# Optimization experiments

Hardware: AMD Instinct MI355X
Metric: run time of the kernel (lower is better)

Reference implementation:

```python
import jax, jax.numpy as jnp
import numpy as np

WIN_H, WIN_W = 8, 8
NUM_HEADS = 32


def _relative_position_index(wh: int, ww: int) -> np.ndarray:
    # Swin V1 style pairwise relative position index, [wh*ww, wh*ww]
    coords = np.stack(np.meshgrid(np.arange(wh), np.arange(ww), indexing='ij'))  # [2, wh, ww]
    cf = coords.reshape(2, -1)                      # [2, N]
    rel = cf[:, :, None] - cf[:, None, :]           # [2, N, N]
    rel = rel.transpose(1, 2, 0).copy()             # [N, N, 2]
    rel[:, :, 0] += wh - 1
    rel[:, :, 1] += ww - 1
    rel[:, :, 0] *= 2 * ww - 1
    return rel.sum(-1)                              # [N, N]


def setup_inputs() -> dict:
    key = jax.random.key(0)
    ks = jax.random.split(key, 6)
    B, N, C = 2048, WIN_H * WIN_W, 256
    return {
        'x': jax.random.normal(ks[0], (B, N, C), dtype=jnp.float32),
        'w_qkv': jax.random.normal(ks[1], (3 * C, C), dtype=jnp.float32) * 0.02,
        'b_qkv': jax.random.normal(ks[2], (3 * C,), dtype=jnp.float32) * 0.02,
        'w_proj': jax.random.normal(ks[3], (C, C), dtype=jnp.float32) * 0.02,
        'b_proj': jax.random.normal(ks[4], (C,), dtype=jnp.float32) * 0.02,
        'bias_table': jax.random.normal(ks[5], ((2 * WIN_H - 1) * (2 * WIN_W - 1), NUM_HEADS), dtype=jnp.float32) * 0.02,
    }


def reference(x, w_qkv, b_qkv, w_proj, b_proj, bias_table):
    B, N, C = x.shape
    H = NUM_HEADS
    d = C // H
    idx = jnp.asarray(_relative_position_index(WIN_H, WIN_W).reshape(-1))  # [N*N] int
    # gathered relative positional bias: [H, N, N]
    bias = bias_table[idx].reshape(N, N, H).transpose(2, 0, 1)
    # qkv projection -> [3, B, H, N, d]
    qkv = (x @ w_qkv.T + b_qkv).reshape(B, N, 3, H, d).transpose(2, 0, 3, 1, 4)
    q, k, v = qkv[0], qkv[1], qkv[2]
    # NOTE: torch code normalizes over dim=1 == HEAD axis (faithful quirk),
    # and self.scale is never applied in forward.
    def norm_heads(t):
        n = jnp.sqrt(jnp.sum(t * t, axis=1, keepdims=True))
        return t / jnp.maximum(n, 1e-12)
    q = norm_heads(q)
    k = norm_heads(k)
    logits = jnp.einsum('bhqd,bhkd->bhqk', q, k) + bias[None]  # [B,H,N,N]
    attn = jax.nn.softmax(logits, axis=-1)
    out = jnp.einsum('bhqk,bhkd->bhqd', attn, v)               # [B,H,N,d]
    out = out.transpose(0, 2, 1, 3).reshape(B, N, C)
    return out @ w_proj.T + b_proj
```

## Files before the change

kernel.cpp:

```cpp
#include <hip/hip_runtime.h>

typedef __attribute__((ext_vector_type(4))) float f32x4;
typedef __attribute__((ext_vector_type(8))) short s16x8;
typedef __attribute__((ext_vector_type(4))) short s16x4;

#define NWIN 2048
#define NTOK 64
#define CDIM 256
#define NHEAD 32

__device__ __forceinline__ ushort f2bf(float f) {
    union { float f; unsigned u; } v; v.f = f;
    unsigned r = v.u + 0x7FFFu + ((v.u >> 16) & 1u);
    return (ushort)(r >> 16);
}
__device__ __forceinline__ float bf2f(ushort u) {
    union { unsigned u; float f; } v; v.u = ((unsigned)u) << 16;
    return v.f;
}

__global__ void prep_kernel(const float* __restrict__ wqkv,
                            const float* __restrict__ wproj,
                            const float* __restrict__ btab,
                            ushort* __restrict__ wq,
                            ushort* __restrict__ wp,
                            ushort* __restrict__ bb) {
    int t = blockIdx.x * 256 + threadIdx.x;
    if (t < 196608) {
        wq[t] = f2bf(wqkv[t]);
    } else if (t < 262144) {
        int i = t - 196608;
        wp[i] = f2bf(wproj[i]);
    } else if (t < 393216) {
        int i = t - 262144;
        int h  = i >> 12;
        int rem = i & 4095;
        int qi = rem >> 6;
        int kj = rem & 63;
        int rh = (qi >> 3) - (kj >> 3) + 7;
        int rw = (qi & 7)  - (kj & 7)  + 7;
        bb[i] = f2bf(btab[(rh * 15 + rw) * 32 + h]);
    }
}

__global__ __launch_bounds__(512, 2) void attn_kernel(
    const float* __restrict__ x,
    const float* __restrict__ bqkv,
    const float* __restrict__ bproj,
    const ushort* __restrict__ wq,
    const ushort* __restrict__ wp,
    const ushort* __restrict__ biasb,
    float* __restrict__ out)
{
    __shared__ ushort sQ [NHEAD * NTOK * 8];
    __shared__ ushort sK [NHEAD * NTOK * 8];
    __shared__ ushort sVT[NHEAD * 8 * NTOK];
    __shared__ ushort sX [NTOK * CDIM];

    const int tid  = threadIdx.x;
    const int lane = tid & 63;
    const int w    = tid >> 6;
    const int g    = lane >> 4;
    const int c    = lane & 15;
    const int b    = blockIdx.x;

    const f32x4 fz = {0.f, 0.f, 0.f, 0.f};
    const s16x4 sz4 = {0, 0, 0, 0};

    {
        const float4* xg = (const float4*)(x + (size_t)b * (NTOK * CDIM));
        #pragma unroll
        for (int it = 0; it < 8; ++it) {
            int i = tid + it * 512;
            float4 v = xg[i];
            int row = i >> 6;
            int col = (i & 63) << 2;
            int bo = row * 512 + col * 2;
            bo ^= (row & 7) << 4;
            ushort4 u;
            u.x = f2bf(v.x); u.y = f2bf(v.y); u.z = f2bf(v.z); u.w = f2bf(v.w);
            *(ushort4*)((char*)sX + bo) = u;
        }
    }
    __syncthreads();

    {
        f32x4 acc[4][6];
        #pragma unroll
        for (int mi = 0; mi < 4; ++mi)
            #pragma unroll
            for (int nj = 0; nj < 6; ++nj) acc[mi][nj] = fz;

        #pragma unroll
        for (int ks = 0; ks < 8; ++ks) {
            s16x8 af[4];
            #pragma unroll
            for (int mi = 0; mi < 4; ++mi) {
                int row = 16 * mi + c;
                int bo = row * 512 + ks * 64 + g * 16;
                bo ^= (row & 7) << 4;
                af[mi] = *(const s16x8*)((const char*)sX + bo);
            }
            s16x8 wfr[6];
            #pragma unroll
            for (int nj = 0; nj < 6; ++nj) {
                int col = 96 * w + 16 * nj + c;
                wfr[nj] = *(const s16x8*)(wq + col * 256 + ks * 32 + g * 8);
            }
            #pragma unroll
            for (int mi = 0; mi < 4; ++mi)
                #pragma unroll
                for (int nj = 0; nj < 6; ++nj)
                    acc[mi][nj] = __builtin_amdgcn_mfma_f32_16x16x32_bf16(
                        af[mi], wfr[nj], acc[mi][nj], 0, 0, 0);
        }

        #pragma unroll
        for (int nj = 0; nj < 6; ++nj) {
            int col   = 96 * w + 16 * nj + c;
            int which = col >> 8;
            int hh    = (col >> 3) & 31;
            int dd    = col & 7;
            float bias = bqkv[col];
            #pragma unroll
            for (int mi = 0; mi < 4; ++mi) {
                #pragma unroll
                for (int j = 0; j < 4; ++j) {
                    int m = 16 * mi + 4 * g + j;
                    ushort bv = f2bf(acc[mi][nj][j] + bias);
                    if (which == 0)      sQ [(hh * 64 + m) * 8 + dd] = bv;
                    else if (which == 1) sK [(hh * 64 + m) * 8 + dd] = bv;
                    else                 sVT[(hh * 8 + dd) * 64 + m] = bv;
                }
            }
        }
    }
    __syncthreads();

    {
        float* sInv = (float*)sX;
        int n = tid >> 3, dd = tid & 7;
        float sq = 0.f, sk = 0.f;
        #pragma unroll 8
        for (int h = 0; h < 32; ++h) {
            float qv = bf2f(sQ[(h * 64 + n) * 8 + dd]);
            float kv = bf2f(sK[(h * 64 + n) * 8 + dd]);
            sq += qv * qv;
            sk += kv * kv;
        }
        sInv[tid]       = 1.f / fmaxf(sqrtf(sq), 1e-12f);
        sInv[512 + tid] = 1.f / fmaxf(sqrtf(sk), 1e-12f);
        __syncthreads();
        for (int r = tid; r < 2048; r += 512) {
            int h = r >> 6, nn = r & 63;
            ushort* qp = sQ + (h * 64 + nn) * 8;
            ushort* kp = sK + (h * 64 + nn) * 8;
            const float* iq = sInv + nn * 8;
            const float* ik = sInv + 512 + nn * 8;
            #pragma unroll
            for (int d2 = 0; d2 < 8; ++d2) {
                qp[d2] = f2bf(bf2f(qp[d2]) * iq[d2]);
                kp[d2] = f2bf(bf2f(kp[d2]) * ik[d2]);
            }
        }
    }
    __syncthreads();

    {
        #pragma unroll 1
        for (int hi = 0; hi < 4; ++hi) {
            int h = w * 4 + hi;
            s16x4 kf[4], qf[4];
            #pragma unroll
            for (int t = 0; t < 4; ++t) {
                if (g < 2) {
                    kf[t] = *(const s16x4*)(sK + (h * 64 + 16 * t + c) * 8 + g * 4);
                    qf[t] = *(const s16x4*)(sQ + (h * 64 + 16 * t + c) * 8 + g * 4);
                } else { kf[t] = sz4; qf[t] = sz4; }
            }
            f32x4 S[4][4];
            #pragma unroll
            for (int tk = 0; tk < 4; ++tk)
                #pragma unroll
                for (int tq = 0; tq < 4; ++tq)
                    S[tk][tq] = __builtin_amdgcn_mfma_f32_16x16x16bf16_1k(
                        kf[tk], qf[tq], fz, 0, 0, 0);

            const ushort* bh = biasb + h * 4096;
            float rinv[4];
            #pragma unroll
            for (int tq = 0; tq < 4; ++tq) {
                float sum = 0.f;
                #pragma unroll
                for (int tk = 0; tk < 4; ++tk) {
                    ushort4 bv4 = *(const ushort4*)(bh + (16 * tq + c) * 64 + 16 * tk + 4 * g);
                    float e0 = __expf(S[tk][tq][0] + bf2f(bv4.x));
                    float e1 = __expf(S[tk][tq][1] + bf2f(bv4.y));
                    float e2 = __expf(S[tk][tq][2] + bf2f(bv4.z));
                    float e3 = __expf(S[tk][tq][3] + bf2f(bv4.w));
                    S[tk][tq][0] = e0; S[tk][tq][1] = e1;
                    S[tk][tq][2] = e2; S[tk][tq][3] = e3;
                    sum += e0 + e1 + e2 + e3;
                }
                sum += __shfl_xor(sum, 16);
                sum += __shfl_xor(sum, 32);
                rinv[tq] = 1.f / sum;
            }

            s16x4 vf[4];
            #pragma unroll
            for (int kv = 0; kv < 4; ++kv) {
                if (c < 8) vf[kv] = *(const s16x4*)(sVT + (h * 8 + c) * 64 + 16 * kv + 4 * g);
                else vf[kv] = sz4;
            }
            f32x4 o[4];
            #pragma unroll
            for (int tq = 0; tq < 4; ++tq) o[tq] = fz;
            #pragma unroll
            for (int tq = 0; tq < 4; ++tq) {
                #pragma unroll
                for (int kv = 0; kv < 4; ++kv) {
                    s16x4 pa;
                    pa[0] = (short)f2bf(S[kv][tq][0] * rinv[tq]);
                    pa[1] = (short)f2bf(S[kv][tq][1] * rinv[tq]);
                    pa[2] = (short)f2bf(S[kv][tq][2] * rinv[tq]);
                    pa[3] = (short)f2bf(S[kv][tq][3] * rinv[tq]);
                    o[tq] = __builtin_amdgcn_mfma_f32_16x16x16bf16_1k(pa, vf[kv], o[tq], 0, 0, 0);
                }
            }
            if (c < 8) {
                #pragma unroll
                for (int tq = 0; tq < 4; ++tq) {
                    #pragma unroll
                    for (int j = 0; j < 4; ++j) {
                        int q = 16 * tq + 4 * g + j;
                        int bo = q * 512 + (h * 8 + c) * 2;
                        bo ^= (q & 7) << 4;
                        *(ushort*)((char*)sX + bo) = f2bf(o[tq][j]);
                    }
                }
            }
        }
    }
    __syncthreads();

    {
        f32x4 pacc[4][2];
        #pragma unroll
        for (int mi = 0; mi < 4; ++mi) { pacc[mi][0] = fz; pacc[mi][1] = fz; }

        #pragma unroll
        for (int ks = 0; ks < 8; ++ks) {
            s16x8 af[4];
            #pragma unroll
            for (int mi = 0; mi < 4; ++mi) {
                int row = 16 * mi + c;
                int bo = row * 512 + ks * 64 + g * 16;
                bo ^= (row & 7) << 4;
                af[mi] = *(const s16x8*)((const char*)sX + bo);
            }
            s16x8 wfr[2];
            #pragma unroll
            for (int nj = 0; nj < 2; ++nj) {
                int col = 32 * w + 16 * nj + c;
                wfr[nj] = *(const s16x8*)(wp + col * 256 + ks * 32 + g * 8);
            }
            #pragma unroll
            for (int mi = 0; mi < 4; ++mi)
                #pragma unroll
                for (int nj = 0; nj < 2; ++nj)
                    pacc[mi][nj] = __builtin_amdgcn_mfma_f32_16x16x32_bf16(
                        af[mi], wfr[nj], pacc[mi][nj], 0, 0, 0);
        }

        float* og = out + (size_t)b * (NTOK * CDIM);
        #pragma unroll
        for (int nj = 0; nj < 2; ++nj) {
            int col = 32 * w + 16 * nj + c;
            float bp = bproj[col];
            #pragma unroll
            for (int mi = 0; mi < 4; ++mi) {
                #pragma unroll
                for (int j = 0; j < 4; ++j) {
                    int row = 16 * mi + 4 * g + j;
                    og[row * 256 + col] = pacc[mi][nj][j] + bp;
                }
            }
        }
    }
}

extern "C" void kernel_launch(void* const* d_in, const int* in_sizes, int n_in,
                              void* d_out, int out_size, void* d_ws, size_t ws_size,
                              hipStream_t stream) {
    const float* x     = (const float*)d_in[0];
    const float* wqkv  = (const float*)d_in[1];
    const float* bqkv  = (const float*)d_in[2];
    const float* wproj = (const float*)d_in[3];
    const float* bproj = (const float*)d_in[4];
    const float* btab  = (const float*)d_in[5];

    ushort* wq_b   = (ushort*)d_ws;
    ushort* wp_b   = wq_b + 196608;
    ushort* bias_b = wp_b + 65536;

    prep_kernel<<<1536, 256, 0, stream>>>(wqkv, wproj, btab, wq_b, wp_b, bias_b);
    attn_kernel<<<NWIN, 512, 0, stream>>>(x, bqkv, bproj, wq_b, wp_b, bias_b,
                                          (float*)d_out);
}
```

Baseline: 361.0 us.

## Keep Q/K/V in registers and drop shared staging buffers

Q, K and V projections now stay in registers. Each wave computes the head slices it later consumes, with Q/K computed transposed so the accumulator layout matches the MFMA operand layout. The head-axis norm is accumulated with shared-memory atomicAdd into a small buffer, which removes the sQ/sK/sVT arrays and the separate normalisation pass with its extra barrier. The smaller LDS footprint allows launch bounds of 4 blocks per CU. The cost is higher register pressure from many live accumulators, plus LDS atomic contention.

```diff
diff --git a/kernel.cpp b/kernel.cpp
--- a/kernel.cpp
+++ b/kernel.cpp
@@ -5,9 +5,6 @@
 typedef __attribute__((ext_vector_type(4))) short s16x4;
 
 #define NWIN 2048
-#define NTOK 64
-#define CDIM 256
-#define NHEAD 32
 
 __device__ __forceinline__ ushort f2bf(float f) {
     union { float f; unsigned u; } v; v.f = f;
@@ -18,6 +15,10 @@
     union { unsigned u; float f; } v; v.u = ((unsigned)u) << 16;
     return v.f;
 }
+__device__ __forceinline__ unsigned pk2(float a, float b) {
+    return (unsigned)f2bf(a) | ((unsigned)f2bf(b) << 16);
+}
+union BF4 { unsigned u[2]; s16x4 v; };
 
 __global__ void prep_kernel(const float* __restrict__ wqkv,
                             const float* __restrict__ wproj,
@@ -43,7 +44,7 @@
     }
 }
 
-__global__ __launch_bounds__(512, 2) void attn_kernel(
+__global__ __launch_bounds__(512, 4) void attn_kernel(
     const float* __restrict__ x,
     const float* __restrict__ bqkv,
     const float* __restrict__ bproj,
@@ -52,10 +53,8 @@
     const ushort* __restrict__ biasb,
     float* __restrict__ out)
 {
-    __shared__ ushort sQ [NHEAD * NTOK * 8];
-    __shared__ ushort sK [NHEAD * NTOK * 8];
-    __shared__ ushort sVT[NHEAD * 8 * NTOK];
-    __shared__ ushort sX [NTOK * CDIM];
+    __shared__ ushort sX[64 * 256];
+    __shared__ float  sN[1024];
 
     const int tid  = threadIdx.x;
     const int lane = tid & 63;
@@ -65,18 +64,19 @@
     const int b    = blockIdx.x;
 
     const f32x4 fz = {0.f, 0.f, 0.f, 0.f};
-    const s16x4 sz4 = {0, 0, 0, 0};
+    const s16x4 z4 = {0, 0, 0, 0};
+
+    sN[tid] = 0.f; sN[tid + 512] = 0.f;
 
     {
-        const float4* xg = (const float4*)(x + (size_t)b * (NTOK * CDIM));
+        const float4* xg = (const float4*)(x + (size_t)b * 16384);
         #pragma unroll
         for (int it = 0; it < 8; ++it) {
             int i = tid + it * 512;
             float4 v = xg[i];
             int row = i >> 6;
             int col = (i & 63) << 2;
-            int bo = row * 512 + col * 2;
-            bo ^= (row & 7) << 4;
+            int bo = (row * 512 + col * 2) ^ ((row & 7) << 4);
             ushort4 u;
             u.x = f2bf(v.x); u.y = f2bf(v.y); u.z = f2bf(v.z); u.w = f2bf(v.w);
             *(ushort4*)((char*)sX + bo) = u;
@@ -84,159 +84,170 @@
     }
     __syncthreads();
 
+    unsigned vpku[4][2][2];
     {
-        f32x4 acc[4][6];
-        #pragma unroll
-        for (int mi = 0; mi < 4; ++mi)
-            #pragma unroll
-            for (int nj = 0; nj < 6; ++nj) acc[mi][nj] = fz;
-
+        f32x4 acc[4][2];
+        #pragma unroll
+        for (int mi = 0; mi < 4; ++mi) { acc[mi][0] = fz; acc[mi][1] = fz; }
         #pragma unroll
         for (int ks = 0; ks < 8; ++ks) {
             s16x8 af[4];
             #pragma unroll
             for (int mi = 0; mi < 4; ++mi) {
                 int row = 16 * mi + c;
-                int bo = row * 512 + ks * 64 + g * 16;
-                bo ^= (row & 7) << 4;
+                int bo = (row * 512 + ks * 64 + g * 16) ^ ((row & 7) << 4);
                 af[mi] = *(const s16x8*)((const char*)sX + bo);
             }
-            s16x8 wfr[6];
-            #pragma unroll
-            for (int nj = 0; nj < 6; ++nj) {
-                int col = 96 * w + 16 * nj + c;
-                wfr[nj] = *(const s16x8*)(wq + col * 256 + ks * 32 + g * 8);
-            }
+            s16x8 wv[2];
+            #pragma unroll
+            for (int nj = 0; nj < 2; ++nj)
+                wv[nj] = *(const s16x8*)(wq + (512 + 32 * w + 16 * nj + c) * 256 + ks * 32 + g * 8);
             #pragma unroll
             for (int mi = 0; mi < 4; ++mi)
                 #pragma unroll
-                for (int nj = 0; nj < 6; ++nj)
-                    acc[mi][nj] = __builtin_amdgcn_mfma_f32_16x16x32_bf16(
-                        af[mi], wfr[nj], acc[mi][nj], 0, 0, 0);
-        }
-
-        #pragma unroll
-        for (int nj = 0; nj < 6; ++nj) {
-            int col   = 96 * w + 16 * nj + c;
-            int which = col >> 8;
-            int hh    = (col >> 3) & 31;
-            int dd    = col & 7;
-            float bias = bqkv[col];
-            #pragma unroll
-            for (int mi = 0; mi < 4; ++mi) {
-                #pragma unroll
-                for (int j = 0; j < 4; ++j) {
-                    int m = 16 * mi + 4 * g + j;
-                    ushort bv = f2bf(acc[mi][nj][j] + bias);
-                    if (which == 0)      sQ [(hh * 64 + m) * 8 + dd] = bv;
-                    else if (which == 1) sK [(hh * 64 + m) * 8 + dd] = bv;
-                    else                 sVT[(hh * 8 + dd) * 64 + m] = bv;
+                for (int nj = 0; nj < 2; ++nj)
+                    acc[mi][nj] = __builtin_amdgcn_mfma_f32_16x16x32_bf16(af[mi], wv[nj], acc[mi][nj], 0, 0, 0);
+        }
+        float bv[2];
+        bv[0] = bqkv[512 + 32 * w + c];
+        bv[1] = bqkv[512 + 32 * w + 16 + c];
+        #pragma unroll
+        for (int mi = 0; mi < 4; ++mi)
+            #pragma unroll
+            for (int nj = 0; nj < 2; ++nj) {
+                vpku[mi][nj][0] = pk2(acc[mi][nj][0] + bv[nj], acc[mi][nj][1] + bv[nj]);
+                vpku[mi][nj][1] = pk2(acc[mi][nj][2] + bv[nj], acc[mi][nj][3] + bv[nj]);
+            }
+    }
+
+    f32x4 aq[2][4], ak[2][4];
+    {
+        #pragma unroll
+        for (int mt = 0; mt < 2; ++mt)
+            #pragma unroll
+            for (int nt = 0; nt < 4; ++nt) { aq[mt][nt] = fz; ak[mt][nt] = fz; }
+        #pragma unroll
+        for (int ks = 0; ks < 8; ++ks) {
+            s16x8 af[4];
+            #pragma unroll
+            for (int nt = 0; nt < 4; ++nt) {
+                int row = 16 * nt + c;
+                int bo = (row * 512 + ks * 64 + g * 16) ^ ((row & 7) << 4);
+                af[nt] = *(const s16x8*)((const char*)sX + bo);
+            }
+            s16x8 wqa[2], wka[2];
+            #pragma unroll
+            for (int mt = 0; mt < 2; ++mt) {
+                wqa[mt] = *(const s16x8*)(wq + (32 * w + 16 * mt + c) * 256 + ks * 32 + g * 8);
+                wka[mt] = *(const s16x8*)(wq + (256 + 32 * w + 16 * mt + c) * 256 + ks * 32 + g * 8);
+            }
+            #pragma unroll
+            for (int mt = 0; mt < 2; ++mt)
+                #pragma unroll
+                for (int nt = 0; nt < 4; ++nt) {
+                    aq[mt][nt] = __builtin_amdgcn_mfma_f32_16x16x32_bf16(wqa[mt], af[nt], aq[mt][nt], 0, 0, 0);
+                    ak[mt][nt] = __builtin_amdgcn_mfma_f32_16x16x32_bf16(wka[mt], af[nt], ak[mt][nt], 0, 0, 0);
                 }
-            }
-        }
+        }
+        f32x4 bq[2], bk[2];
+        bq[0] = *(const f32x4*)(bqkv + 32 * w + 4 * g);
+        bq[1] = *(const f32x4*)(bqkv + 32 * w + 16 + 4 * g);
+        bk[0] = *(const f32x4*)(bqkv + 256 + 32 * w + 4 * g);
+        bk[1] = *(const f32x4*)(bqkv + 256 + 32 * w + 16 + 4 * g);
+        #pragma unroll
+        for (int mt = 0; mt < 2; ++mt)
+            #pragma unroll
+            for (int nt = 0; nt < 4; ++nt) { aq[mt][nt] += bq[mt]; ak[mt][nt] += bk[mt]; }
+        #pragma unroll
+        for (int nt = 0; nt < 4; ++nt)
+            #pragma unroll
+            for (int j = 0; j < 4; ++j) {
+                int a = (16 * nt + c) * 8 + ((4 * g + j) & 7);
+                atomicAdd(&sN[a],       aq[0][nt][j] * aq[0][nt][j] + aq[1][nt][j] * aq[1][nt][j]);
+                atomicAdd(&sN[a + 512], ak[0][nt][j] * ak[0][nt][j] + ak[1][nt][j] * ak[1][nt][j]);
+            }
     }
     __syncthreads();
 
-    {
-        float* sInv = (float*)sX;
-        int n = tid >> 3, dd = tid & 7;
-        float sq = 0.f, sk = 0.f;
-        #pragma unroll 8
-        for (int h = 0; h < 32; ++h) {
-            float qv = bf2f(sQ[(h * 64 + n) * 8 + dd]);
-            float kv = bf2f(sK[(h * 64 + n) * 8 + dd]);
-            sq += qv * qv;
-            sk += kv * kv;
-        }
-        sInv[tid]       = 1.f / fmaxf(sqrtf(sq), 1e-12f);
-        sInv[512 + tid] = 1.f / fmaxf(sqrtf(sk), 1e-12f);
-        __syncthreads();
-        for (int r = tid; r < 2048; r += 512) {
-            int h = r >> 6, nn = r & 63;
-            ushort* qp = sQ + (h * 64 + nn) * 8;
-            ushort* kp = sK + (h * 64 + nn) * 8;
-            const float* iq = sInv + nn * 8;
-            const float* ik = sInv + 512 + nn * 8;
-            #pragma unroll
-            for (int d2 = 0; d2 < 8; ++d2) {
-                qp[d2] = f2bf(bf2f(qp[d2]) * iq[d2]);
-                kp[d2] = f2bf(bf2f(kp[d2]) * ik[d2]);
-            }
-        }
-    }
-    __syncthreads();
-
-    {
-        #pragma unroll 1
-        for (int hi = 0; hi < 4; ++hi) {
-            int h = w * 4 + hi;
-            s16x4 kf[4], qf[4];
-            #pragma unroll
-            for (int t = 0; t < 4; ++t) {
-                if (g < 2) {
-                    kf[t] = *(const s16x4*)(sK + (h * 64 + 16 * t + c) * 8 + g * 4);
-                    qf[t] = *(const s16x4*)(sQ + (h * 64 + 16 * t + c) * 8 + g * 4);
-                } else { kf[t] = sz4; qf[t] = sz4; }
-            }
-            f32x4 S[4][4];
-            #pragma unroll
-            for (int tk = 0; tk < 4; ++tk)
-                #pragma unroll
-                for (int tq = 0; tq < 4; ++tq)
-                    S[tk][tq] = __builtin_amdgcn_mfma_f32_16x16x16bf16_1k(
-                        kf[tk], qf[tq], fz, 0, 0, 0);
-
-            const ushort* bh = biasb + h * 4096;
-            float rinv[4];
-            #pragma unroll
-            for (int tq = 0; tq < 4; ++tq) {
+    s16x4 qpk[2][4], kpk[2][4];
+    #pragma unroll
+    for (int nt = 0; nt < 4; ++nt) {
+        float iq[4], ik[4];
+        #pragma unroll
+        for (int j = 0; j < 4; ++j) {
+            int a = (16 * nt + c) * 8 + ((4 * g + j) & 7);
+            iq[j] = 1.f / fmaxf(sqrtf(sN[a]), 1e-12f);
+            ik[j] = 1.f / fmaxf(sqrtf(sN[a + 512]), 1e-12f);
+        }
+        #pragma unroll
+        for (int mt = 0; mt < 2; ++mt) {
+            BF4 uq, uk;
+            uq.u[0] = pk2(aq[mt][nt][0] * iq[0], aq[mt][nt][1] * iq[1]);
+            uq.u[1] = pk2(aq[mt][nt][2] * iq[2], aq[mt][nt][3] * iq[3]);
+            uk.u[0] = pk2(ak[mt][nt][0] * ik[0], ak[mt][nt][1] * ik[1]);
+            uk.u[1] = pk2(ak[mt][nt][2] * ik[2], ak[mt][nt][3] * ik[3]);
+            qpk[mt][nt] = uq.v; kpk[mt][nt] = uk.v;
+        }
+    }
+
+    #pragma unroll
+    for (int hi = 0; hi < 4; ++hi) {
+        const int mt = hi >> 1, par = hi & 1, h = 4 * w + hi;
+        const bool keepq = par ? (g >= 2) : (g < 2);
+        s16x4 vf[4];
+        #pragma unroll
+        for (int kv = 0; kv < 4; ++kv) {
+            unsigned u0 = vpku[kv][mt][0], u1 = vpku[kv][mt][1];
+            if (par) { u0 = (unsigned)__shfl_xor((int)u0, 8); u1 = (unsigned)__shfl_xor((int)u1, 8); }
+            BF4 t; t.u[0] = u0; t.u[1] = u1;
+            vf[kv] = (c < 8) ? t.v : z4;
+        }
+        const ushort* bh = biasb + h * 4096;
+        #pragma unroll
+        for (int tqh = 0; tqh < 2; ++tqh) {
+            f32x4 S[4][2];
+            #pragma unroll
+            for (int t2 = 0; t2 < 2; ++t2) {
+                s16x4 qf = keepq ? qpk[mt][2 * tqh + t2] : z4;
+                #pragma unroll
+                for (int tk = 0; tk < 4; ++tk)
+                    S[tk][t2] = __builtin_amdgcn_mfma_f32_16x16x16bf16_1k(kpk[mt][tk], qf, fz, 0, 0, 0);
+            }
+            float rinv[2];
+            #pragma unroll
+            for (int t2 = 0; t2 < 2; ++t2) {
                 float sum = 0.f;
                 #pragma unroll
                 for (int tk = 0; tk < 4; ++tk) {
-                    ushort4 bv4 = *(const ushort4*)(bh + (16 * tq + c) * 64 + 16 * tk + 4 * g);
-                    float e0 = __expf(S[tk][tq][0] + bf2f(bv4.x));
-                    float e1 = __expf(S[tk][tq][1] + bf2f(bv4.y));
-                    float e2 = __expf(S[tk][tq][2] + bf2f(bv4.z));
-                    float e3 = __expf(S[tk][tq][3] + bf2f(bv4.w));
-                    S[tk][tq][0] = e0; S[tk][tq][1] = e1;
-                    S[tk][tq][2] = e2; S[tk][tq][3] = e3;
+                    ushort4 bv4 = *(const ushort4*)(bh + (16 * (2 * tqh + t2) + c) * 64 + 16 * tk + 4 * g);
+                    float e0 = __expf(S[tk][t2][0] + bf2f(bv4.x));
+                    float e1 = __expf(S[tk][t2][1] + bf2f(bv4.y));
+                    float e2 = __expf(S[tk][t2][2] + bf2f(bv4.z));
+                    float e3 = __expf(S[tk][t2][3] + bf2f(bv4.w));
+                    S[tk][t2][0] = e0; S[tk][t2][1] = e1;
+                    S[tk][t2][2] = e2; S[tk][t2][3] = e3;
                     sum += e0 + e1 + e2 + e3;
                 }
                 sum += __shfl_xor(sum, 16);
                 sum += __shfl_xor(sum, 32);
-                rinv[tq] = 1.f / sum;
-            }
-
-            s16x4 vf[4];
-            #pragma unroll
-            for (int kv = 0; kv < 4; ++kv) {
-                if (c < 8) vf[kv] = *(const s16x4*)(sVT + (h * 8 + c) * 64 + 16 * kv + 4 * g);
-                else vf[kv] = sz4;
-            }
-            f32x4 o[4];
-            #pragma unroll
-            for (int tq = 0; tq < 4; ++tq) o[tq] = fz;
-            #pragma unroll
-            for (int tq = 0; tq < 4; ++tq) {
+                rinv[t2] = 1.f / sum;
+            }
+            #pragma unroll
+            for (int t2 = 0; t2 < 2; ++t2) {
+                f32x4 o = fz;
                 #pragma unroll
                 for (int kv = 0; kv < 4; ++kv) {
-                    s16x4 pa;
-                    pa[0] = (short)f2bf(S[kv][tq][0] * rinv[tq]);
-                    pa[1] = (short)f2bf(S[kv][tq][1] * rinv[tq]);
-                    pa[2] = (short)f2bf(S[kv][tq][2] * rinv[tq]);
-                    pa[3] = (short)f2bf(S[kv][tq][3] * rinv[tq]);
-                    o[tq] = __builtin_amdgcn_mfma_f32_16x16x16bf16_1k(pa, vf[kv], o[tq], 0, 0, 0);
+                    BF4 pa;
+                    pa.u[0] = pk2(S[kv][t2][0] * rinv[t2], S[kv][t2][1] * rinv[t2]);
+                    pa.u[1] = pk2(S[kv][t2][2] * rinv[t2], S[kv][t2][3] * rinv[t2]);
+                    o = __builtin_amdgcn_mfma_f32_16x16x16bf16_1k(pa.v, vf[kv], o, 0, 0, 0);
                 }
-            }
-            if (c < 8) {
-                #pragma unroll
-                for (int tq = 0; tq < 4; ++tq) {
+                if (c < 8) {
                     #pragma unroll
                     for (int j = 0; j < 4; ++j) {
-                        int q = 16 * tq + 4 * g + j;
-                        int bo = q * 512 + (h * 8 + c) * 2;
-                        bo ^= (q & 7) << 4;
-                        *(ushort*)((char*)sX + bo) = f2bf(o[tq][j]);
+                        int tok = 16 * (2 * tqh + t2) + 4 * g + j;
+                        int bo = (tok * 512 + (h * 8 + c) * 2) ^ ((tok & 7) << 4);
+                        *(ushort*)((char*)sX + bo) = f2bf(o[j]);
                     }
                 }
             }
@@ -248,44 +259,35 @@
         f32x4 pacc[4][2];
         #pragma unroll
         for (int mi = 0; mi < 4; ++mi) { pacc[mi][0] = fz; pacc[mi][1] = fz; }
-
         #pragma unroll
         for (int ks = 0; ks < 8; ++ks) {
             s16x8 af[4];
             #pragma unroll
             for (int mi = 0; mi < 4; ++mi) {
                 int row = 16 * mi + c;
-                int bo = row * 512 + ks * 64 + g * 16;
-                bo ^= (row & 7) << 4;
+                int bo = (row * 512 + ks * 64 + g * 16) ^ ((row & 7) << 4);
                 af[mi] = *(const s16x8*)((const char*)sX + bo);
             }
             s16x8 wfr[2];
             #pragma unroll
-            for (int nj = 0; nj < 2; ++nj) {
-                int col = 32 * w + 16 * nj + c;
-                wfr[nj] = *(const s16x8*)(wp + col * 256 + ks * 32 + g * 8);
-            }
+            for (int nj = 0; nj < 2; ++nj)
+                wfr[nj] = *(const s16x8*)(wp + (32 * w + 16 * nj + c) * 256 + ks * 32 + g * 8);
             #pragma unroll
             for (int mi = 0; mi < 4; ++mi)
                 #pragma unroll
                 for (int nj = 0; nj < 2; ++nj)
-                    pacc[mi][nj] = __builtin_amdgcn_mfma_f32_16x16x32_bf16(
-                        af[mi], wfr[nj], pacc[mi][nj], 0, 0, 0);
-        }
-
-        float* og = out + (size_t)b * (NTOK * CDIM);
+                    pacc[mi][nj] = __builtin_amdgcn_mfma_f32_16x16x32_bf16(af[mi], wfr[nj], pacc[mi][nj], 0, 0, 0);
+        }
+        float* og = out + (size_t)b * 16384;
         #pragma unroll
         for (int nj = 0; nj < 2; ++nj) {
             int col = 32 * w + 16 * nj + c;
             float bp = bproj[col];
             #pragma unroll
-            for (int mi = 0; mi < 4; ++mi) {
-                #pragma unroll
-                for (int j = 0; j < 4; ++j) {
-                    int row = 16 * mi + 4 * g + j;
-                    og[row * 256 + col] = pacc[mi][nj][j] + bp;
-                }
-            }
+            for (int mi = 0; mi < 4; ++mi)
+                #pragma unroll
+                for (int j = 0; j < 4; ++j)
+                    og[(16 * mi + 4 * g + j) * 256 + col] = pacc[mi][nj][j] + bp;
         }
     }
 }
```

Result: slower. 650.6 us (+80.2%).
